# Optimization experiments

Measured on AMD Instinct MI355X. Metric: run time of the kernel, lower is better.

## Reference

```python
import jax, jax.numpy as jnp
import numpy as np
import math

D = 512; H = 4; HD = 128; S = 100; B = 32
HIN, WIN = 143, 111
HOUT, WOUT = 135, 103
FLAT = HIN * WIN  # 15873


def _pe():
    pos = np.arange(S, dtype=np.float32)[:, None]
    div = np.exp(np.arange(0, D, 2, dtype=np.float32) * (-math.log(10000.0) / D))
    pe = np.zeros((S, D), dtype=np.float32)
    pe[:, 0::2] = np.sin(pos * div)
    pe[:, 1::2] = np.cos(pos * div)
    return jnp.asarray(pe[:, None, :])  # (S,1,D)


def _pool_mat(n_in, n_out):
    # PyTorch AdaptiveAvgPool semantics: window [floor(i*in/out), ceil((i+1)*in/out))
    M = np.zeros((n_out, n_in), dtype=np.float32)
    for i in range(n_out):
        s = (i * n_in) // n_out
        e = -((-(i + 1) * n_in) // n_out)
        M[i, s:e] = 1.0 / (e - s)
    return jnp.asarray(M)


def _ln(x, g, b, eps=1e-5):
    m = jnp.mean(x, -1, keepdims=True)
    v = jnp.mean((x - m) ** 2, -1, keepdims=True)
    return (x - m) * jax.lax.rsqrt(v + eps) * g + b


def _mha(q_in, kv_in, qkv_w, qkv_b, pw, pb, key_pad):
    # q_in: (Sq,B,D), kv_in: (Sk,B,D); seq-first like nn.Transformer
    q = q_in @ qkv_w[:D].T + qkv_b[:D]
    k = kv_in @ qkv_w[D:2 * D].T + qkv_b[D:2 * D]
    v = kv_in @ qkv_w[2 * D:].T + qkv_b[2 * D:]
    Sq, Bb = q.shape[0], q.shape[1]
    Sk = k.shape[0]
    q = q.reshape(Sq, Bb, H, HD)
    k = k.reshape(Sk, Bb, H, HD)
    v = v.reshape(Sk, Bb, H, HD)
    sc = jnp.einsum('qbhd,kbhd->bhqk', q, k) / math.sqrt(HD)
    if key_pad is not None:
        sc = jnp.where(key_pad[:, None, None, :], -1e9, sc)
    a = jax.nn.softmax(sc, -1)
    o = jnp.einsum('bhqk,kbhd->qbhd', a, v).reshape(Sq, Bb, D)
    return o @ pw.T + pb


def _forward(x, fc1_w, fc1_b, fc2_w, fc2_b, fc3_w, fc3_b,
             out1_w, out1_b, out2_w, out2_b, out3_w, out3_b,
             enc_qkv_w, enc_qkv_b, enc_proj_w, enc_proj_b,
             enc_ff1_w, enc_ff1_b, enc_ff2_w, enc_ff2_b,
             enc_ln1_g, enc_ln1_b, enc_ln2_g, enc_ln2_b, enc_lnf_g, enc_lnf_b,
             dec_sa_qkv_w, dec_sa_qkv_b, dec_sa_proj_w, dec_sa_proj_b,
             dec_ca_qkv_w, dec_ca_qkv_b, dec_ca_proj_w, dec_ca_proj_b,
             dec_ff1_w, dec_ff1_b, dec_ff2_w, dec_ff2_b,
             dec_ln1_g, dec_ln1_b, dec_ln2_g, dec_ln2_b, dec_ln3_g, dec_ln3_b,
             dec_lnf_g, dec_lnf_b):
    Bb = x.shape[0]
    # Vectorized replacement of the per-sample torch.nonzero double loop:
    # padding[b,i] = True iff all timesteps k >= i are all-zero (and i >= 1).
    nz = jnp.any(x != 0, axis=(2, 3))  # (B,S)
    suffix_any = jnp.flip(jnp.cumsum(jnp.flip(nz, 1).astype(jnp.int32), 1), 1) > 0
    padding = (~suffix_any).at[:, 0].set(False)  # torch loop never touches step 0

    h = x.reshape(Bb * S, FLAT)
    h = jax.nn.relu(h @ fc1_w.T + fc1_b)
    h = jax.nn.relu(h @ fc2_w.T + fc2_b)
    h = jax.nn.relu(h @ fc3_w.T + fc3_b)
    h = h.reshape(Bb, S, D).transpose(1, 0, 2) + _pe()  # (S,B,D)

    for i in range(2):  # encoder, post-norm
        a = _mha(h, h, enc_qkv_w[i], enc_qkv_b[i], enc_proj_w[i], enc_proj_b[i], padding)
        h = _ln(h + a, enc_ln1_g[i], enc_ln1_b[i])
        f = jax.nn.relu(h @ enc_ff1_w[i].T + enc_ff1_b[i]) @ enc_ff2_w[i].T + enc_ff2_b[i]
        h = _ln(h + f, enc_ln2_g[i], enc_ln2_b[i])
    memory = _ln(h, enc_lnf_g, enc_lnf_b)

    t = jnp.ones((1, Bb, D), jnp.float32)  # trg
    for i in range(2):  # decoder, post-norm
        a = _mha(t, t, dec_sa_qkv_w[i], dec_sa_qkv_b[i], dec_sa_proj_w[i], dec_sa_proj_b[i], None)
        t = _ln(t + a, dec_ln1_g[i], dec_ln1_b[i])
        a = _mha(t, memory, dec_ca_qkv_w[i], dec_ca_qkv_b[i], dec_ca_proj_w[i], dec_ca_proj_b[i], None)
        t = _ln(t + a, dec_ln2_g[i], dec_ln2_b[i])
        f = jax.nn.relu(t @ dec_ff1_w[i].T + dec_ff1_b[i]) @ dec_ff2_w[i].T + dec_ff2_b[i]
        t = _ln(t + f, dec_ln3_g[i], dec_ln3_b[i])
    t = _ln(t, dec_lnf_g, dec_lnf_b)

    o = t[0]  # (B,512)
    o = jax.nn.relu(o @ out1_w.T + out1_b)
    o = jax.nn.relu(o @ out2_w.T + out2_b)
    o = jax.nn.relu(o @ out3_w.T + out3_b)
    o = o.reshape(Bb, HIN, WIN)
    return jnp.einsum('oh,bhw,pw->bop', _pool_mat(HIN, HOUT), o, _pool_mat(WIN, WOUT))


def setup_inputs() -> dict:
    key = jax.random.key(0)
    it = iter(jax.random.split(key, 48))

    def w(shape):
        return jax.random.normal(next(it), shape, jnp.float32) * 0.02

    x = jax.random.normal(next(it), (B, S, HIN, WIN), jnp.float32)
    lengths = jax.random.randint(next(it), (B,), 1, S + 1)
    keep = (jnp.arange(S)[None, :] < lengths[:, None]).astype(jnp.float32)
    x = x * keep[:, :, None, None]  # ragged: trailing timesteps are all-zero

    z, o1 = jnp.zeros, jnp.ones
    return dict(
        x=x,
        fc1_w=w((4096, FLAT)), fc1_b=z(4096),
        fc2_w=w((2048, 4096)), fc2_b=z(2048),
        fc3_w=w((D, 2048)), fc3_b=z(D),
        out1_w=w((2048, D)), out1_b=z(2048),
        out2_w=w((4096, 2048)), out2_b=z(4096),
        out3_w=w((FLAT, 4096)), out3_b=z(FLAT),
        enc_qkv_w=w((2, 3 * D, D)), enc_qkv_b=z((2, 3 * D)),
        enc_proj_w=w((2, D, D)), enc_proj_b=z((2, D)),
        enc_ff1_w=w((2, 1024, D)), enc_ff1_b=z((2, 1024)),
        enc_ff2_w=w((2, D, 1024)), enc_ff2_b=z((2, D)),
        enc_ln1_g=o1((2, D)), enc_ln1_b=z((2, D)),
        enc_ln2_g=o1((2, D)), enc_ln2_b=z((2, D)),
        enc_lnf_g=o1(D), enc_lnf_b=z(D),
        dec_sa_qkv_w=w((2, 3 * D, D)), dec_sa_qkv_b=z((2, 3 * D)),
        dec_sa_proj_w=w((2, D, D)), dec_sa_proj_b=z((2, D)),
        dec_ca_qkv_w=w((2, 3 * D, D)), dec_ca_qkv_b=z((2, 3 * D)),
        dec_ca_proj_w=w((2, D, D)), dec_ca_proj_b=z((2, D)),
        dec_ff1_w=w((2, 1024, D)), dec_ff1_b=z((2, 1024)),
        dec_ff2_w=w((2, D, 1024)), dec_ff2_b=z((2, D)),
        dec_ln1_g=o1((2, D)), dec_ln1_b=z((2, D)),
        dec_ln2_g=o1((2, D)), dec_ln2_b=z((2, D)),
        dec_ln3_g=o1((2, D)), dec_ln3_b=z((2, D)),
        dec_lnf_g=o1(D), dec_lnf_b=z(D),
    )


def reference(x, fc1_w, fc1_b, fc2_w, fc2_b, fc3_w, fc3_b,
              out1_w, out1_b, out2_w, out2_b, out3_w, out3_b,
              enc_qkv_w, enc_qkv_b, enc_proj_w, enc_proj_b,
              enc_ff1_w, enc_ff1_b, enc_ff2_w, enc_ff2_b,
              enc_ln1_g, enc_ln1_b, enc_ln2_g, enc_ln2_b, enc_lnf_g, enc_lnf_b,
              dec_sa_qkv_w, dec_sa_qkv_b, dec_sa_proj_w, dec_sa_proj_b,
              dec_ca_qkv_w, dec_ca_qkv_b, dec_ca_proj_w, dec_ca_proj_b,
              dec_ff1_w, dec_ff1_b, dec_ff2_w, dec_ff2_b,
              dec_ln1_g, dec_ln1_b, dec_ln2_g, dec_ln2_b, dec_ln3_g, dec_ln3_b,
              dec_lnf_g, dec_lnf_b):
    return _forward(x, fc1_w, fc1_b, fc2_w, fc2_b, fc3_w, fc3_b,
                    out1_w, out1_b, out2_w, out2_b, out3_w, out3_b,
                    enc_qkv_w, enc_qkv_b, enc_proj_w, enc_proj_b,
                    enc_ff1_w, enc_ff1_b, enc_ff2_w, enc_ff2_b,
                    enc_ln1_g, enc_ln1_b, enc_ln2_g, enc_ln2_b, enc_lnf_g, enc_lnf_b,
                    dec_sa_qkv_w, dec_sa_qkv_b, dec_sa_proj_w, dec_sa_proj_b,
                    dec_ca_qkv_w, dec_ca_qkv_b, dec_ca_proj_w, dec_ca_proj_b,
                    dec_ff1_w, dec_ff1_b, dec_ff2_w, dec_ff2_b,
                    dec_ln1_g, dec_ln1_b, dec_ln2_g, dec_ln2_b, dec_ln3_g, dec_ln3_b,
                    dec_lnf_g, dec_lnf_b)
```

## Files before the change

kernel.cpp:

```cpp
#include <hip/hip_runtime.h>
#include <hip/hip_bf16.h>

#define SEQ   100
#define BATCH 32
#define FLATIN 15873
#define KPAD1  16384
#define ROWS   3200
#define MPAD   3328
#define NOUT3  16000

typedef __attribute__((ext_vector_type(8))) short short8;
typedef __attribute__((ext_vector_type(4))) short short4v;
typedef __attribute__((ext_vector_type(4))) float f32x4;
typedef __hip_bfloat16 bf16;

__device__ __forceinline__ void gload_lds16(const void* g, void* l) {
  __builtin_amdgcn_global_load_lds((const __attribute__((address_space(1))) void*)g,
                                   (__attribute__((address_space(3))) void*)l, 16, 0, 0);
}

__device__ __forceinline__ int xcd_swizzle(int id, int nwg) {
  const int q = nwg >> 3, r = nwg & 7;
  const int x = id & 7, p = id >> 3;
  return (x < r ? x * (q + 1) : r * (q + 1) + (x - r) * q) + p;
}

#define GEMM_BODY(KBEG, KEND)                                                   \
  const int tid  = threadIdx.x;                                                 \
  const int lane = tid & 63;                                                    \
  const int wid  = tid >> 6;                                                    \
  const int wr = (wid >> 1) << 6;                                               \
  const int wc = (wid & 1) << 6;                                                \
  f32x4 acc[4][4];                                                              \
  _Pragma("unroll") for (int i = 0; i < 4; ++i)                                 \
  _Pragma("unroll") for (int j = 0; j < 4; ++j)                                 \
      acc[i][j] = (f32x4){0.f, 0.f, 0.f, 0.f};                                  \
  const int srow = (wid << 3) + (lane >> 3);                                    \
  const int scs  = lane & 7;                                                    \
  const int gcol = ((scs ^ (srow & 7)) << 3);                                   \
  const bf16* arow[4];                                                          \
  const bf16* brow[4];                                                          \
  _Pragma("unroll") for (int j = 0; j < 4; ++j) {                               \
    const int row = (j << 5) + srow;                                            \
    const int gr = GATHER ? idx[m0 + row] : (m0 + row);                         \
    arow[j] = A + (size_t)gr * K + gcol;                                        \
    brow[j] = W + (size_t)(n0 + row) * K + gcol;                                \
  }                                                                             \
  for (int k0 = (KBEG); k0 < (KEND); k0 += 64) {                                \
    __syncthreads();                                                            \
    _Pragma("unroll") for (int j = 0; j < 4; ++j) {                             \
      short* la = As + (((j << 2) + wid) << 9);                                 \
      short* lb = Bs + (((j << 2) + wid) << 9);                                 \
      gload_lds16(arow[j] + k0, la);                                            \
      gload_lds16(brow[j] + k0, lb);                                            \
    }                                                                           \
    __syncthreads();                                                            \
    _Pragma("unroll") for (int kk = 0; kk < 2; ++kk) {                          \
      short8 af[4], bfv[4];                                                     \
      _Pragma("unroll") for (int i = 0; i < 4; ++i) {                           \
        const int mr = wr + (i << 4) + (lane & 15);                             \
        const int cg = (kk << 2) + (lane >> 4);                                 \
        af[i]  = *(const short8*)(As + mr * 64 + ((cg ^ (mr & 7)) << 3));       \
        const int nr = wc + (i << 4) + (lane & 15);                             \
        bfv[i] = *(const short8*)(Bs + nr * 64 + ((cg ^ (nr & 7)) << 3));       \
      }                                                                         \
      _Pragma("unroll") for (int i = 0; i < 4; ++i)                             \
      _Pragma("unroll") for (int j = 0; j < 4; ++j)                             \
          acc[i][j] = __builtin_amdgcn_mfma_f32_16x16x32_bf16(af[i], bfv[j],    \
                                                              acc[i][j], 0,0,0);\
    }                                                                           \
  }

template<int GATHER>
__global__ __launch_bounds__(256)
void gemm_bf16(const bf16* __restrict__ A, const bf16* __restrict__ W,
               const int* __restrict__ idx, const int* __restrict__ cnt,
               float* __restrict__ P,
               int K, int ldc, int mtiles, int ksl, size_t pstride)
{
  __shared__ __align__(16) short lds[16384];
  short* As = lds;
  short* Bs = lds + 8192;
  const int wg = xcd_swizzle(blockIdx.x, gridDim.x);
  const int mt = wg % mtiles;
  const int g  = wg / mtiles;
  const int nt = g / ksl;
  const int ks = g % ksl;
  const int m0 = mt << 7;
  const int n0 = nt << 7;
  if (cnt && m0 >= cnt[0]) return;
  const int Klen = K / ksl;
  const int kbeg = ks * Klen;

  GEMM_BODY(kbeg, kbeg + Klen)

  float* Pout = P + (size_t)ks * pstride;
  const int fr = lane & 15, fq = lane >> 4;
#pragma unroll
  for (int j = 0; j < 4; ++j) {
    const int n = n0 + wc + (j << 4) + fr;
#pragma unroll
    for (int i = 0; i < 4; ++i)
#pragma unroll
      for (int r = 0; r < 4; ++r) {
        const int m = m0 + wr + (i << 4) + (fq << 2) + r;
        Pout[(size_t)m * ldc + n] = acc[i][j][r];
      }
  }
}

template<int RELU, int OF32, int OB16>
__global__ __launch_bounds__(256)
void gemm_direct(const bf16* __restrict__ A, const bf16* __restrict__ W,
                 const float* __restrict__ bias, float* __restrict__ Cf,
                 bf16* __restrict__ Cb, int K, int ldc, int mtiles)
{
  __shared__ __align__(16) short lds[16384];
  short* As = lds;
  short* Bs = lds + 8192;
  const int GATHER = 0;
  const int* idx = nullptr;
  const int wg = xcd_swizzle(blockIdx.x, gridDim.x);
  const int m0 = (wg % mtiles) << 7;
  const int n0 = (wg / mtiles) << 7;

  GEMM_BODY(0, K)

  const int fr = lane & 15, fq = lane >> 4;
#pragma unroll
  for (int j = 0; j < 4; ++j) {
    const int n = n0 + wc + (j << 4) + fr;
    const float bb = bias[n];
#pragma unroll
    for (int i = 0; i < 4; ++i)
#pragma unroll
      for (int r = 0; r < 4; ++r) {
        const int m = m0 + wr + (i << 4) + (fq << 2) + r;
        float v = acc[i][j][r] + bb;
        if (RELU) v = fmaxf(v, 0.f);
        if (OF32) Cf[(size_t)m * ldc + n] = v;
        if (OB16) Cb[(size_t)m * ldc + n] = __float2bfloat16(v);
      }
  }
}

__global__ __launch_bounds__(256)
void gemm_w32(const bf16* __restrict__ A, const float* __restrict__ W32,
              float* __restrict__ P, int K, int ldc, int ksl, size_t pstride,
              int wrows)
{
  __shared__ __align__(16) short lds[16384];
  short* As = lds;
  short* Bs = lds + 8192;
  const int wg = xcd_swizzle(blockIdx.x, gridDim.x);
  const int nt = wg / ksl;
  const int ks = wg % ksl;
  const int m0 = 0;
  const int n0 = nt << 7;
  const int Klen = K / ksl;
  const int kbeg = ks * Klen;
  const int kend = kbeg + Klen;

  const int tid  = threadIdx.x;
  const int lane = tid & 63;
  const int wid  = tid >> 6;
  const int wr = (wid >> 1) << 6;
  const int wc = (wid & 1) << 6;

  f32x4 acc[4][4];
#pragma unroll
  for (int i = 0; i < 4; ++i)
#pragma unroll
    for (int j = 0; j < 4; ++j) acc[i][j] = (f32x4){0.f, 0.f, 0.f, 0.f};

  const int srow = (wid << 3) + (lane >> 3);
  const int scs  = lane & 7;
  const int gcol = ((scs ^ (srow & 7)) << 3);

  const bf16* arow[4];
#pragma unroll
  for (int j = 0; j < 4; ++j)
    arow[j] = A + (size_t)(m0 + (j << 5) + srow) * K + gcol;

  const float* wsrc[4];
  int bslot[4];
#pragma unroll
  for (int i = 0; i < 4; ++i) {
    const int q = (i << 8) + tid;
    const int row = q >> 3, c = q & 7;
    const int wrow = min(n0 + row, wrows - 1);
    wsrc[i] = W32 + (size_t)wrow * K + (c << 3);
    bslot[i] = row * 64 + ((c ^ (row & 7)) << 3);
  }

  for (int k0 = kbeg; k0 < kend; k0 += 64) {
    __syncthreads();
#pragma unroll
    for (int j = 0; j < 4; ++j)
      gload_lds16(arow[j] + k0, As + (((j << 2) + wid) << 9));
#pragma unroll
    for (int i = 0; i < 4; ++i) {
      const float4 w0 = *(const float4*)(wsrc[i] + k0);
      const float4 w1 = *(const float4*)(wsrc[i] + k0 + 4);
      union { short8 v; bf16 h[8]; } pk;
      pk.h[0] = __float2bfloat16(w0.x); pk.h[1] = __float2bfloat16(w0.y);
      pk.h[2] = __float2bfloat16(w0.z); pk.h[3] = __float2bfloat16(w0.w);
      pk.h[4] = __float2bfloat16(w1.x); pk.h[5] = __float2bfloat16(w1.y);
      pk.h[6] = __float2bfloat16(w1.z); pk.h[7] = __float2bfloat16(w1.w);
      *(short8*)(Bs + bslot[i]) = pk.v;
    }
    __syncthreads();
#pragma unroll
    for (int kk = 0; kk < 2; ++kk) {
      short8 af[4], bfv[4];
#pragma unroll
      for (int i = 0; i < 4; ++i) {
        const int mr = wr + (i << 4) + (lane & 15);
        const int cg = (kk << 2) + (lane >> 4);
        af[i]  = *(const short8*)(As + mr * 64 + ((cg ^ (mr & 7)) << 3));
        const int nr = wc + (i << 4) + (lane & 15);
        bfv[i] = *(const short8*)(Bs + nr * 64 + ((cg ^ (nr & 7)) << 3));
      }
#pragma unroll
      for (int i = 0; i < 4; ++i)
#pragma unroll
        for (int j = 0; j < 4; ++j)
          acc[i][j] = __builtin_amdgcn_mfma_f32_16x16x32_bf16(af[i], bfv[j], acc[i][j], 0, 0, 0);
    }
  }

  float* Pout = P + (size_t)ks * pstride;
  const int fr = lane & 15, fq = lane >> 4;
#pragma unroll
  for (int j = 0; j < 4; ++j) {
    const int n = n0 + wc + (j << 4) + fr;
#pragma unroll
    for (int i = 0; i < 4; ++i)
#pragma unroll
      for (int r = 0; r < 4; ++r) {
        const int m = m0 + wr + (i << 4) + (fq << 2) + r;
        Pout[(size_t)m * ldc + n] = acc[i][j][r];
      }
  }
}

template<int RELU, int OF32, int OB16>
__global__ __launch_bounds__(256)
void reduce_kernel(const float* __restrict__ P, size_t pstride, int ksl,
                   const float* __restrict__ bias, float* __restrict__ Cf,
                   bf16* __restrict__ Cb, int N, const int* __restrict__ cnt)
{
  const int row = blockIdx.y;
  if (cnt) { const int cp = (cnt[0] + 127) & ~127; if (row >= cp) return; }
  const int n = (blockIdx.x * 256 + threadIdx.x) * 4;
  if (n >= N) return;
  const size_t o = (size_t)row * N + n;
  const float4 b4 = *(const float4*)(bias + n);
  float4 s = *(const float4*)(P + o);
  for (int k = 1; k < ksl; ++k) {
    const float4 p = *(const float4*)(P + (size_t)k * pstride + o);
    s.x += p.x; s.y += p.y; s.z += p.z; s.w += p.w;
  }
  s.x += b4.x; s.y += b4.y; s.z += b4.z; s.w += b4.w;
  if (RELU) {
    s.x = fmaxf(s.x, 0.f); s.y = fmaxf(s.y, 0.f);
    s.z = fmaxf(s.z, 0.f); s.w = fmaxf(s.w, 0.f);
  }
  if (OF32) *(float4*)(Cf + o) = s;
  if (OB16) {
    union { short4v v; bf16 h[4]; } u;
    u.h[0] = __float2bfloat16(s.x);
    u.h[1] = __float2bfloat16(s.y);
    u.h[2] = __float2bfloat16(s.z);
    u.h[3] = __float2bfloat16(s.w);
    *(short4v*)(Cb + o) = u.v;
  }
}

__global__ __launch_bounds__(256)
void conv_x_kernel(const float* __restrict__ x, bf16* __restrict__ xb,
                   int* __restrict__ nz)
{
  __shared__ int sred[4];
  const int m = blockIdx.x;
  const int t = threadIdx.x;
  bf16* dst = xb + (size_t)m * KPAD1;
  if (m == ROWS) {
    const __hip_bfloat162 z2 = {__float2bfloat16(0.f), __float2bfloat16(0.f)};
    for (int c = t; c < (KPAD1 >> 1); c += 256) *(__hip_bfloat162*)(dst + 2 * c) = z2;
    return;
  }
  const float* src = x + (size_t)m * FLATIN;
  int any = 0;
  for (int c = t; c < (KPAD1 >> 1); c += 256) {
    const int c0 = 2 * c;
    const float v0 = (c0 < FLATIN) ? src[c0] : 0.f;
    const float v1 = (c0 + 1 < FLATIN) ? src[c0 + 1] : 0.f;
    any |= (v0 != 0.f) | (v1 != 0.f);
    __hip_bfloat162 pr;
    pr.x = __float2bfloat16(v0);
    pr.y = __float2bfloat16(v1);
    *(__hip_bfloat162*)(dst + c0) = pr;
  }
  any = __any(any) ? 1 : 0;
  if ((t & 63) == 0) sred[t >> 6] = any;
  __syncthreads();
  if (t == 0) nz[m] = sred[0] | sred[1] | sred[2] | sred[3];
}

__global__ __launch_bounds__(256)
void compact_kernel(const int* __restrict__ nz, int* __restrict__ idx,
                    int* __restrict__ pos, int* __restrict__ cnt,
                    int* __restrict__ pad,
                    const float* __restrict__ dkvb, float* __restrict__ kvbias)
{
  __shared__ int wsum[4];
  __shared__ int total;
  const int t = threadIdx.x;
  int loc[13];
  int c = 0;
#pragma unroll
  for (int i = 0; i < 13; ++i) {
    const int m = t * 13 + i;
    loc[i] = (m < ROWS) ? nz[m] : 0;
    c += loc[i];
  }
  int v = c;
#pragma unroll
  for (int o = 1; o < 64; o <<= 1) {
    const int u = __shfl_up(v, o);
    if ((t & 63) >= o) v += u;
  }
  if ((t & 63) == 63) wsum[t >> 6] = v;
  __syncthreads();
  int wbase = 0;
  for (int w = 0; w < (t >> 6); ++w) wbase += wsum[w];
  int p = wbase + v - c;
#pragma unroll
  for (int i = 0; i < 13; ++i) {
    const int m = t * 13 + i;
    if (m < ROWS) {
      if (loc[i]) { idx[p] = m; pos[m] = p; ++p; }
      else pos[m] = -1;
    }
  }
  if (t == 255) total = p;
  __syncthreads();
  const int count = total;
  if (t == 0) cnt[0] = count + 1;
  for (int i = count + t; i < MPAD; i += 256) idx[i] = ROWS;
  for (int m = t; m < ROWS; m += 256) if (pos[m] < 0) pos[m] = count;
  if (t < 32) {
    int any = 0;
    for (int s = 99; s >= 0; --s) {
      any |= nz[t * 100 + s];
      pad[t * 100 + s] = (s > 0 && !any) ? 1 : 0;
    }
  }
#pragma unroll
  for (int i = t; i < 2048; i += 256) {
    const int L = i >> 10, j = i & 1023;
    kvbias[i] = dkvb[L * 1536 + 512 + j];
  }
}

struct CvtArgs {
  const float* src[8];
  bf16* dst[8];
  int cum[8];
};
struct TrArgs {
  const float* src[13];
  float* dst[13];
  int R[13], C[13], cum[13];
};
struct PrepArgs {
  CvtArgs cv;
  TrArgs tr;
  const float* fc1w;
  bf16* wb1;
  int nCvt, nFc1;
};
__global__ __launch_bounds__(256)
void prep_kernel(PrepArgs a)
{
  __shared__ float tbuf[64][65];
  const int bid0 = blockIdx.x;
  if (bid0 < a.nCvt) {
    const int bid = bid0;
    int seg = 0;
#pragma unroll
    for (int i = 1; i < 8; ++i) if (bid >= a.cv.cum[i]) seg = i;
    const size_t e0 = ((size_t)(bid - a.cv.cum[seg]) << 11) + (threadIdx.x << 3);
    const float4 v0 = *(const float4*)(a.cv.src[seg] + e0);
    const float4 v1 = *(const float4*)(a.cv.src[seg] + e0 + 4);
    union { short8 v; bf16 h[8]; } pk;
    pk.h[0] = __float2bfloat16(v0.x); pk.h[1] = __float2bfloat16(v0.y);
    pk.h[2] = __float2bfloat16(v0.z); pk.h[3] = __float2bfloat16(v0.w);
    pk.h[4] = __float2bfloat16(v1.x); pk.h[5] = __float2bfloat16(v1.y);
    pk.h[6] = __float2bfloat16(v1.z); pk.h[7] = __float2bfloat16(v1.w);
    *(short8*)(a.cv.dst[seg] + e0) = pk.v;
  } else if (bid0 < a.nCvt + a.nFc1) {
    const int r = bid0 - a.nCvt;
    const float* src = a.fc1w + (size_t)r * FLATIN;
    bf16* dst = a.wb1 + (size_t)r * KPAD1;
#pragma unroll
    for (int u = 0; u < KPAD1 / 2048; ++u) {
      const int c0 = u * 2048 + threadIdx.x * 8;
      union { short8 v; bf16 h[8]; } pk;
      if (c0 + 8 <= FLATIN) {
        const float4 p = *(const float4*)(src + c0);
        const float4 q = *(const float4*)(src + c0 + 4);
        pk.h[0] = __float2bfloat16(p.x); pk.h[1] = __float2bfloat16(p.y);
        pk.h[2] = __float2bfloat16(p.z); pk.h[3] = __float2bfloat16(p.w);
        pk.h[4] = __float2bfloat16(q.x); pk.h[5] = __float2bfloat16(q.y);
        pk.h[6] = __float2bfloat16(q.z); pk.h[7] = __float2bfloat16(q.w);
      } else {
#pragma unroll
        for (int i = 0; i < 8; ++i)
          pk.h[i] = __float2bfloat16((c0 + i < FLATIN) ? src[c0 + i] : 0.f);
      }
      *(short8*)(dst + c0) = pk.v;
    }
  } else {
    const int bid = bid0 - a.nCvt - a.nFc1;
    int seg = 0;
#pragma unroll
    for (int i = 1; i < 13; ++i) if (bid >= a.tr.cum[i]) seg = i;
    const int local = bid - a.tr.cum[seg];
    const int R = a.tr.R[seg], C = a.tr.C[seg];
    const int tilesC = C >> 6;
    const int r0 = (local / tilesC) << 6;
    const int c0 = (local % tilesC) << 6;
    const int tx = threadIdx.x & 63, ty = threadIdx.x >> 6;
    const float* s = a.tr.src[seg];
    float* d = a.tr.dst[seg];
#pragma unroll
    for (int i = 0; i < 16; ++i) {
      const int rr = (ty << 4) + i;
      tbuf[rr][tx] = s[(size_t)(r0 + rr) * C + c0 + tx];
    }
    __syncthreads();
#pragma unroll
    for (int i = 0; i < 16; ++i) {
      const int cc = (ty << 4) + i;
      d[(size_t)(c0 + cc) * R + r0 + tx] = tbuf[tx][cc];
    }
  }
}

__global__ __launch_bounds__(256)
void scatter_pe_reduce(const float* __restrict__ P, size_t pstride, int ksl,
                       const int* __restrict__ pos, const float* __restrict__ bias,
                       float* __restrict__ hf, bf16* __restrict__ hb)
{
  const int m = blockIdx.x;
  const int s = m % 100, b = m / 100;
  const int src = pos[m];
  const int t = threadIdx.x;
  const size_t sb = (size_t)src * 512;
  const size_t db = (size_t)(s * 32 + b) * 512;
#pragma unroll
  for (int u = 0; u < 2; ++u) {
    const int d = t + u * 256;
    float v = bias[d];
    for (int k = 0; k < ksl; ++k) v += P[(size_t)k * pstride + sb + d];
    const float div = expf((float)(2 * (d >> 1)) * (-9.210340371976184f / 512.f));
    const float arg = (float)s * div;
    const float pe = (d & 1) ? cosf(arg) : sinf(arg);
    v = fmaxf(v, 0.f) + pe;
    hf[db + d] = v;
    hb[db + d] = __float2bfloat16(v);
  }
}

__global__ __launch_bounds__(256)
void ln_kernel(const float* __restrict__ x, const float* __restrict__ res,
               const float* __restrict__ g, const float* __restrict__ bta,
               const float* __restrict__ gf, const float* __restrict__ bf_,
               int dofinal, float* __restrict__ y, bf16* __restrict__ yb)
{
  __shared__ float rs[4], rss[4];
  const int row = blockIdx.x;
  const int t = threadIdx.x;
  const size_t base = (size_t)row * 512;
  float v0 = x[base + t];
  float v1 = x[base + t + 256];
  if (res) { v0 += res[base + t]; v1 += res[base + t + 256]; }
  float o0, o1;
#pragma unroll
  for (int pass = 0; pass < 2; ++pass) {
    float s = v0 + v1, ss = v0 * v0 + v1 * v1;
#pragma unroll
    for (int o = 32; o > 0; o >>= 1) { s += __shfl_xor(s, o); ss += __shfl_xor(ss, o); }
    if ((t & 63) == 0) { rs[t >> 6] = s; rss[t >> 6] = ss; }
    __syncthreads();
    s = rs[0] + rs[1] + rs[2] + rs[3];
    ss = rss[0] + rss[1] + rss[2] + rss[3];
    __syncthreads();
    const float mean = s * (1.f / 512.f);
    const float var = ss * (1.f / 512.f) - mean * mean;
    const float inv = rsqrtf(var + 1e-5f);
    const float* gg = (pass == 0) ? g : gf;
    const float* bb = (pass == 0) ? bta : bf_;
    o0 = (v0 - mean) * inv * gg[t] + bb[t];
    o1 = (v1 - mean) * inv * gg[t + 256] + bb[t + 256];
    if (pass == 1 || !dofinal) break;
    v0 = o0; v1 = o1;
  }
  if (y) {
    y[base + t] = o0;
    y[base + t + 256] = o1;
  }
  if (yb) {
    yb[base + t] = __float2bfloat16(o0);
    yb[base + t + 256] = __float2bfloat16(o1);
  }
}

__global__ __launch_bounds__(256)
void enc_attn_kernel(const float* __restrict__ qkv, const int* __restrict__ pad,
                     bf16* __restrict__ ob)
{
  __shared__ float Ks[100][129];
  __shared__ float Qs[128];
  __shared__ float Ps[100];
  __shared__ float red[4];
  const int bh = blockIdx.x;
  const int b = bh >> 2, h = bh & 3;
  const int q0 = blockIdx.y * 4;
  const int t = threadIdx.x;
  for (int i = t; i < 12800; i += 256) {
    const int s = i >> 7, d = i & 127;
    Ks[s][d] = qkv[(size_t)(s * 32 + b) * 1536 + 512 + h * 128 + d];
  }
  const int masked = (t < 100) ? pad[b * 100 + t] : 0;
  const float scale = 0.08838834764831845f;
  for (int qi = 0; qi < 4; ++qi) {
    const int q = q0 + qi;
    __syncthreads();
    if (t < 128) Qs[t] = qkv[(size_t)(q * 32 + b) * 1536 + h * 128 + t];
    __syncthreads();
    float sc = -3e38f;
    if (t < 100) {
      const float* kr = &Ks[t][0];
      float a = 0.f;
#pragma unroll 16
      for (int d = 0; d < 128; ++d) a += Qs[d] * kr[d];
      sc = masked ? -1e9f : (a * scale);
    }
    float mx = sc;
#pragma unroll
    for (int o = 32; o > 0; o >>= 1) mx = fmaxf(mx, __shfl_xor(mx, o));
    if ((t & 63) == 0) red[t >> 6] = mx;
    __syncthreads();
    mx = fmaxf(fmaxf(red[0], red[1]), fmaxf(red[2], red[3]));
    const float e = (t < 100) ? expf(sc - mx) : 0.f;
    float sm = e;
#pragma unroll
    for (int o = 32; o > 0; o >>= 1) sm += __shfl_xor(sm, o);
    __syncthreads();
    if ((t & 63) == 0) red[t >> 6] = sm;
    __syncthreads();
    sm = red[0] + red[1] + red[2] + red[3];
    if (t < 100) Ps[t] = e;
    __syncthreads();
    if (t < 128) {
      float a = 0.f;
      const float* vb = qkv + 1024 + h * 128 + t;
      for (int k = 0; k < 100; ++k) a += Ps[k] * vb[(size_t)(k * 32 + b) * 1536];
      ob[(size_t)(q * 32 + b) * 512 + h * 128 + t] = __float2bfloat16(a / sm);
    }
  }
}

template<int N, int K, int RELU>
__device__ __forceinline__ void gemvT(int tid, const float* S,
                                      const float* __restrict__ WT,
                                      const float* __restrict__ bias,
                                      float* out, float* part)
{
  constexpr int NQ = N / 4;
  constexpr int G = 512 / NQ;
  constexpr int KP = K / G;
  const int p = tid % NQ;
  const int g = tid / NQ;
  const float4* wp = (const float4*)WT;
  float ax = 0.f, ay = 0.f, az = 0.f, aw = 0.f;
  const int kend = g * KP + KP;
#pragma unroll 8
  for (int k = g * KP; k < kend; ++k) {
    const float s = S[k];
    const float4 w = wp[(size_t)k * NQ + p];
    ax += s * w.x; ay += s * w.y; az += s * w.z; aw += s * w.w;
  }
  float4 a4 = {ax, ay, az, aw};
  *(float4*)(part + g * N + 4 * p) = a4;
  __syncthreads();
#pragma unroll
  for (int n = tid; n < N; n += 512) {
    float v = bias[n];
#pragma unroll
    for (int q = 0; q < G; ++q) v += part[q * N + n];
    if (RELU) v = fmaxf(v, 0.f);
    out[n] = v;
  }
  __syncthreads();
}

#define BLOCK_LN512(V, G, B, O)                                                 \
  {                                                                             \
    float s_ = (V), ss_ = (V) * (V);                                            \
    _Pragma("unroll")                                                           \
    for (int o_ = 32; o_ > 0; o_ >>= 1) {                                       \
      s_ += __shfl_xor(s_, o_); ss_ += __shfl_xor(ss_, o_);                     \
    }                                                                           \
    if ((tid & 63) == 0) { red[tid >> 6] = s_; red2[tid >> 6] = ss_; }          \
    __syncthreads();                                                            \
    s_ = 0.f; ss_ = 0.f;                                                        \
    _Pragma("unroll")                                                           \
    for (int w_ = 0; w_ < 8; ++w_) { s_ += red[w_]; ss_ += red2[w_]; }          \
    const float mean_ = s_ * (1.f / 512.f);                                     \
    const float inv_ = rsqrtf(ss_ * (1.f / 512.f) - mean_ * mean_ + 1e-5f);     \
    O = ((V) - mean_) * inv_ * (G)[tid] + (B)[tid];                             \
    __syncthreads();                                                            \
  }

__global__ __launch_bounds__(512)
void dec_layer(const float* __restrict__ tin,
               const float* __restrict__ kvb, int kvstride,
               const float* __restrict__ WvT, const float* __restrict__ bv,
               const float* __restrict__ WpT, const float* __restrict__ bp,
               const float* __restrict__ g1, const float* __restrict__ b1,
               const float* __restrict__ WqT, const float* __restrict__ bq,
               const float* __restrict__ WcpT, const float* __restrict__ bcp,
               const float* __restrict__ g2, const float* __restrict__ b2,
               const float* __restrict__ W1T, const float* __restrict__ b1f,
               const float* __restrict__ W2T, const float* __restrict__ b2f,
               const float* __restrict__ g3, const float* __restrict__ b3,
               const float* __restrict__ gf, const float* __restrict__ bf_,
               int dofinal, float* __restrict__ tout,
               const float* __restrict__ Wo1T, const float* __restrict__ ob1,
               bf16* __restrict__ o1b)
{
  __shared__ float Ts[512], Bs[512], Cs[512], F1[1024], part[2048];
  __shared__ float Ps[4][104];
  __shared__ float red[8], red2[8];
  const int r = blockIdx.x, tid = threadIdx.x;
  Ts[tid] = tin ? tin[r * 512 + tid] : 1.0f;
  __syncthreads();

  gemvT<512, 512, 0>(tid, Ts, WvT, bv, Bs, part);
  gemvT<512, 512, 0>(tid, Bs, WpT, bp, Cs, part);
  {
    const float rr = Cs[tid] + Ts[tid];
    float o;
    BLOCK_LN512(rr, g1, b1, o)
    Ts[tid] = o;
  }
  __syncthreads();

  gemvT<512, 512, 0>(tid, Ts, WqT, bq, Bs, part);

  if (tid < 256) {
    const int h = tid >> 6, lane = tid & 63;
    const float scale = 0.08838834764831845f;
    const float* Qh = Bs + h * 128;
    float s0, s1 = -3e38f;
    {
      const float* kr = kvb + (size_t)(lane * 32 + r) * kvstride + h * 128;
      float a = 0.f;
#pragma unroll 16
      for (int d = 0; d < 128; ++d) a += Qh[d] * kr[d];
      s0 = a * scale;
    }
    if (lane + 64 < 100) {
      const float* kr = kvb + (size_t)((lane + 64) * 32 + r) * kvstride + h * 128;
      float a = 0.f;
#pragma unroll 16
      for (int d = 0; d < 128; ++d) a += Qh[d] * kr[d];
      s1 = a * scale;
    }
    float mx = fmaxf(s0, s1);
#pragma unroll
    for (int o = 32; o > 0; o >>= 1) mx = fmaxf(mx, __shfl_xor(mx, o));
    const float e0 = expf(s0 - mx);
    const float e1 = (lane + 64 < 100) ? expf(s1 - mx) : 0.f;
    float sm = e0 + e1;
#pragma unroll
    for (int o = 32; o > 0; o >>= 1) sm += __shfl_xor(sm, o);
    Ps[h][lane] = e0 / sm;
    if (lane + 64 < 100) Ps[h][lane + 64] = e1 / sm;
  }
  __syncthreads();
  if (tid < 256) {
    const int h = tid >> 6, lane = tid & 63;
#pragma unroll
    for (int u = 0; u < 2; ++u) {
      const int d = lane + u * 64;
      const float* vb = kvb + 512 + h * 128 + d;
      float a = 0.f;
      for (int k = 0; k < 100; ++k) a += Ps[h][k] * vb[(size_t)(k * 32 + r) * kvstride];
      Bs[h * 128 + d] = a;
    }
  }
  __syncthreads();

  gemvT<512, 512, 0>(tid, Bs, WcpT, bcp, Cs, part);
  {
    const float rr = Cs[tid] + Ts[tid];
    float o;
    BLOCK_LN512(rr, g2, b2, o)
    Ts[tid] = o;
  }
  __syncthreads();

  gemvT<1024, 512, 1>(tid, Ts, W1T, b1f, F1, part);
  gemvT<512, 1024, 0>(tid, F1, W2T, b2f, Cs, part);
  {
    const float rr = Cs[tid] + Ts[tid];
    float o;
    BLOCK_LN512(rr, g3, b3, o)
    if (dofinal) {
      float f;
      BLOCK_LN512(o, gf, bf_, f)
      o = f;
    }
    tout[r * 512 + tid] = o;
    if (dofinal) {
      Ts[tid] = o;
      __syncthreads();
      const float4* wp = (const float4*)Wo1T;
      float ax = 0.f, ay = 0.f, az = 0.f, aw = 0.f;
#pragma unroll 8
      for (int k = 0; k < 512; ++k) {
        const float s = Ts[k];
        const float4 w = wp[(size_t)k * 512 + tid];
        ax += s * w.x; ay += s * w.y; az += s * w.z; aw += s * w.w;
      }
      union { short4v v; bf16 h[4]; } u;
      u.h[0] = __float2bfloat16(fmaxf(ax + ob1[4 * tid], 0.f));
      u.h[1] = __float2bfloat16(fmaxf(ay + ob1[4 * tid + 1], 0.f));
      u.h[2] = __float2bfloat16(fmaxf(az + ob1[4 * tid + 2], 0.f));
      u.h[3] = __float2bfloat16(fmaxf(aw + ob1[4 * tid + 3], 0.f));
      *(short4v*)(o1b + (size_t)r * 2048 + 4 * tid) = u.v;
      const short4v z = {0, 0, 0, 0};
#pragma unroll
      for (int rr = r + 32; rr < 128; rr += 32)
        *(short4v*)(o1b + (size_t)rr * 2048 + 4 * tid) = z;
    }
  }
}

__global__ __launch_bounds__(256)
void reduce_pool(const float* __restrict__ P, size_t pstride,
                 const float* __restrict__ bias, float* __restrict__ out)
{
  __shared__ float row[NOUT3];
  const int b = blockIdx.x, t = threadIdx.x;
  for (int n = t * 4; n < NOUT3; n += 1024) {
    const size_t o = (size_t)b * NOUT3 + n;
    float4 s = *(const float4*)(P + o);
#pragma unroll
    for (int k = 1; k < 4; ++k) {
      const float4 p = *(const float4*)(P + (size_t)k * pstride + o);
      s.x += p.x; s.y += p.y; s.z += p.z; s.w += p.w;
    }
    row[n]     = fmaxf(s.x + ((n     < FLATIN) ? bias[n]     : 0.f), 0.f);
    row[n + 1] = fmaxf(s.y + ((n + 1 < FLATIN) ? bias[n + 1] : 0.f), 0.f);
    row[n + 2] = fmaxf(s.z + ((n + 2 < FLATIN) ? bias[n + 2] : 0.f), 0.f);
    row[n + 3] = fmaxf(s.w + ((n + 3 < FLATIN) ? bias[n + 3] : 0.f), 0.f);
  }
  __syncthreads();
  for (int i = t; i < 135 * 103; i += 256) {
    const int j = i % 103, r = i / 103;
    const int rs = (r * 143) / 135, re = ((r + 1) * 143 + 134) / 135;
    const int cs = (j * 111) / 103, ce = ((j + 1) * 111 + 102) / 103;
    float s = 0.f;
    for (int rr = rs; rr < re; ++rr)
      for (int cc = cs; cc < ce; ++cc)
        s += row[rr * 111 + cc];
    out[(size_t)b * (135 * 103) + i] = s / (float)((re - rs) * (ce - cs));
  }
}

extern "C" void kernel_launch(void* const* d_in, const int* in_sizes, int n_in,
                              void* d_out, int out_size, void* d_ws, size_t ws_size,
                              hipStream_t stream)
{
  (void)in_sizes; (void)n_in; (void)out_size; (void)ws_size;

  const float* x          = (const float*)d_in[0];
  const float* fc1_w      = (const float*)d_in[1];
  const float* fc1_b      = (const float*)d_in[2];
  const float* fc2_w      = (const float*)d_in[3];
  const float* fc2_b      = (const float*)d_in[4];
  const float* fc3_w      = (const float*)d_in[5];
  const float* fc3_b      = (const float*)d_in[6];
  const float* out1_w     = (const float*)d_in[7];
  const float* out1_b     = (const float*)d_in[8];
  const float* out2_w     = (const float*)d_in[9];
  const float* out2_b     = (const float*)d_in[10];
  const float* out3_w     = (const float*)d_in[11];
  const float* out3_b     = (const float*)d_in[12];
  const float* enc_qkv_w  = (const float*)d_in[13];
  const float* enc_qkv_b  = (const float*)d_in[14];
  const float* enc_proj_w = (const float*)d_in[15];
  const float* enc_proj_b = (const float*)d_in[16];
  const float* enc_ff1_w  = (const float*)d_in[17];
  const float* enc_ff1_b  = (const float*)d_in[18];
  const float* enc_ff2_w  = (const float*)d_in[19];
  const float* enc_ff2_b  = (const float*)d_in[20];
  const float* enc_ln1_g  = (const float*)d_in[21];
  const float* enc_ln1_b  = (const float*)d_in[22];
  const float* enc_ln2_g  = (const float*)d_in[23];
  const float* enc_ln2_b  = (const float*)d_in[24];
  const float* enc_lnf_g  = (const float*)d_in[25];
  const float* enc_lnf_b  = (const float*)d_in[26];
  const float* dec_sa_qkv_w  = (const float*)d_in[27];
  const float* dec_sa_qkv_b  = (const float*)d_in[28];
  const float* dec_sa_proj_w = (const float*)d_in[29];
  const float* dec_sa_proj_b = (const float*)d_in[30];
  const float* dec_ca_qkv_w  = (const float*)d_in[31];
  const float* dec_ca_qkv_b  = (const float*)d_in[32];
  const float* dec_ca_proj_w = (const float*)d_in[33];
  const float* dec_ca_proj_b = (const float*)d_in[34];
  const float* dec_ff1_w  = (const float*)d_in[35];
  const float* dec_ff1_b  = (const float*)d_in[36];
  const float* dec_ff2_w  = (const float*)d_in[37];
  const float* dec_ff2_b  = (const float*)d_in[38];
  const float* dec_ln1_g  = (const float*)d_in[39];
  const float* dec_ln1_b  = (const float*)d_in[40];
  const float* dec_ln2_g  = (const float*)d_in[41];
  const float* dec_ln2_b  = (const float*)d_in[42];
  const float* dec_ln3_g  = (const float*)d_in[43];
  const float* dec_ln3_b  = (const float*)d_in[44];
  const float* dec_lnf_g  = (const float*)d_in[45];
  const float* dec_lnf_b  = (const float*)d_in[46];

  char* wsp = (char*)d_ws;
  size_t off = 0;
  auto alloc = [&](size_t nbytes) -> char* {
    char* p = wsp + off;
    off += (nbytes + 255) & ~(size_t)255;
    return p;
  };

  bf16* xb     = (bf16*)alloc((size_t)MPAD * KPAD1 * 2);
  bf16* Wb1    = (bf16*)alloc((size_t)4096 * KPAD1 * 2);
  bf16* Wb2    = (bf16*)alloc((size_t)2048 * 4096 * 2);
  bf16* Wb3    = (bf16*)alloc((size_t)512 * 2048 * 2);
  bf16* Wqkvb  = (bf16*)alloc((size_t)2 * 1536 * 512 * 2);
  bf16* Wprojb = (bf16*)alloc((size_t)2 * 512 * 512 * 2);
  bf16* Wff1b  = (bf16*)alloc((size_t)2 * 1024 * 512 * 2);
  bf16* Wff2b  = (bf16*)alloc((size_t)2 * 512 * 1024 * 2);
  bf16* Wkv2b  = (bf16*)alloc((size_t)2048 * 512 * 2);
  int*   nz      = (int*)alloc(ROWS * 4);
  int*   padmask = (int*)alloc(ROWS * 4);
  int*   idx     = (int*)alloc(MPAD * 4);
  int*   pos     = (int*)alloc(ROWS * 4);
  int*   cnt     = (int*)alloc(256);
  float* kvbias  = (float*)alloc(2048 * 4);
  bf16* h1c = (bf16*)alloc((size_t)MPAD * 4096 * 2);
  bf16* h2c = (bf16*)alloc((size_t)MPAD * 2048 * 2);
  float* hf  = (float*)alloc((size_t)ROWS * 512 * 4);
  bf16* hb = (bf16*)alloc((size_t)ROWS * 512 * 2);
  float* qkvbuf = (float*)alloc((size_t)ROWS * 1536 * 4);
  bf16* attnb = (bf16*)alloc((size_t)ROWS * 512 * 2);
  float* pjf  = (float*)alloc((size_t)ROWS * 512 * 4);
  bf16* f1b = (bf16*)alloc((size_t)ROWS * 1024 * 2);
  float* f2f  = (float*)alloc((size_t)ROWS * 512 * 4);
  bf16* memb = (bf16*)alloc((size_t)ROWS * 512 * 2);
  float* kv01 = (float*)alloc((size_t)ROWS * 2048 * 4);
  float* tbuf = (float*)alloc(32 * 512 * 4);
  float* WvT[2]  = { (float*)alloc(512 * 512 * 4), (float*)alloc(512 * 512 * 4) };
  float* WpT[2]  = { (float*)alloc(512 * 512 * 4), (float*)alloc(512 * 512 * 4) };
  float* WqT[2]  = { (float*)alloc(512 * 512 * 4), (float*)alloc(512 * 512 * 4) };
  float* WcpT[2] = { (float*)alloc(512 * 512 * 4), (float*)alloc(512 * 512 * 4) };
  float* W1T[2]  = { (float*)alloc(512 * 1024 * 4), (float*)alloc(512 * 1024 * 4) };
  float* W2T[2]  = { (float*)alloc(1024 * 512 * 4), (float*)alloc(1024 * 512 * 4) };
  float* Wo1T    = (float*)alloc((size_t)512 * 2048 * 4);
  float* fcP  = (float*)alloc((size_t)4 * MPAD * 4096 * 4);
  float* encP = (float*)alloc((size_t)2 * ROWS * 1536 * 4);

  float* outP = fcP;
  bf16* o1b  = (bf16*)((char*)encP + ((size_t)20 << 20));
  bf16* o2b  = (bf16*)((char*)encP + ((size_t)22 << 20));

  const size_t psF1 = (size_t)MPAD * 4096;
  const size_t psF2 = (size_t)MPAD * 2048;
  const size_t psF3 = (size_t)MPAD * 512;

  conv_x_kernel<<<ROWS + 1, 256, 0, stream>>>(x, xb, nz);
  compact_kernel<<<1, 256, 0, stream>>>(nz, idx, pos, cnt, padmask,
                                        dec_ca_qkv_b, kvbias);
  {
    PrepArgs pa;
    const float* srcs[8] = { enc_qkv_w, enc_proj_w, enc_ff1_w, enc_ff2_w,
                             dec_ca_qkv_w + (size_t)512 * 512,
                             dec_ca_qkv_w + (size_t)(1536 + 512) * 512,
                             fc2_w, fc3_w };
    bf16* dsts[8] = { Wqkvb, Wprojb, Wff1b, Wff2b,
                      Wkv2b, Wkv2b + (size_t)1024 * 512, Wb2, Wb3 };
    const int counts[8] = { 2*1536*512, 2*512*512, 2*1024*512, 2*512*1024,
                            1024*512, 1024*512, 2048*4096, 512*2048 };
    int c = 0;
    for (int i = 0; i < 8; ++i) { pa.cv.src[i] = srcs[i]; pa.cv.dst[i] = dsts[i];
                                  pa.cv.cum[i] = c; c += counts[i] >> 11; }
    pa.nCvt = c;
    pa.fc1w = fc1_w; pa.wb1 = Wb1; pa.nFc1 = 4096;
    const float* tsr[13];
    float* tds[13];
    int R[13], C[13];
    int n = 0;
    for (int L = 0; L < 2; ++L) {
      tsr[n] = dec_sa_qkv_w + (size_t)L * 1536 * 512 + (size_t)1024 * 512;
      tds[n] = WvT[L]; R[n] = 512; C[n] = 512; ++n;
      tsr[n] = dec_sa_proj_w + (size_t)L * 512 * 512;
      tds[n] = WpT[L]; R[n] = 512; C[n] = 512; ++n;
      tsr[n] = dec_ca_qkv_w + (size_t)L * 1536 * 512;
      tds[n] = WqT[L]; R[n] = 512; C[n] = 512; ++n;
      tsr[n] = dec_ca_proj_w + (size_t)L * 512 * 512;
      tds[n] = WcpT[L]; R[n] = 512; C[n] = 512; ++n;
      tsr[n] = dec_ff1_w + (size_t)L * 1024 * 512;
      tds[n] = W1T[L]; R[n] = 1024; C[n] = 512; ++n;
      tsr[n] = dec_ff2_w + (size_t)L * 512 * 1024;
      tds[n] = W2T[L]; R[n] = 512; C[n] = 1024; ++n;
    }
    tsr[n] = out1_w; tds[n] = Wo1T; R[n] = 2048; C[n] = 512; ++n;
    int tc = 0;
    for (int i = 0; i < 13; ++i) {
      pa.tr.src[i] = tsr[i]; pa.tr.dst[i] = tds[i];
      pa.tr.R[i] = R[i]; pa.tr.C[i] = C[i];
      pa.tr.cum[i] = tc; tc += (R[i] >> 6) * (C[i] >> 6);
    }
    prep_kernel<<<pa.nCvt + pa.nFc1 + tc, 256, 0, stream>>>(pa);
  }

  gemm_bf16<1><<<26 * 32 * 2, 256, 0, stream>>>(xb, Wb1, idx, cnt, fcP,
      KPAD1, 4096, 26, 2, psF1);
  reduce_kernel<1, 0, 1><<<dim3(4, MPAD), 256, 0, stream>>>(fcP, psF1, 2,
      fc1_b, nullptr, h1c, 4096, cnt);
  gemm_bf16<0><<<26 * 16 * 4, 256, 0, stream>>>(h1c, Wb2, nullptr, cnt, fcP,
      4096, 2048, 26, 4, psF2);
  reduce_kernel<1, 0, 1><<<dim3(2, MPAD), 256, 0, stream>>>(fcP, psF2, 4,
      fc2_b, nullptr, h2c, 2048, cnt);
  gemm_bf16<0><<<26 * 4 * 4, 256, 0, stream>>>(h2c, Wb3, nullptr, cnt, fcP,
      2048, 512, 26, 4, psF3);
  scatter_pe_reduce<<<ROWS, 256, 0, stream>>>(fcP, psF3, 4, pos, fc3_b, hf, hb);

  for (int L = 0; L < 2; ++L) {
    gemm_direct<0, 1, 0><<<25 * 12, 256, 0, stream>>>(hb, Wqkvb + (size_t)L * 1536 * 512,
        enc_qkv_b + L * 1536, qkvbuf, nullptr, 512, 1536, 25);
    enc_attn_kernel<<<dim3(128, 25), 256, 0, stream>>>(qkvbuf, padmask, attnb);
    gemm_direct<0, 1, 0><<<25 * 4, 256, 0, stream>>>(attnb, Wprojb + (size_t)L * 512 * 512,
        enc_proj_b + L * 512, pjf, nullptr, 512, 512, 25);
    ln_kernel<<<ROWS, 256, 0, stream>>>(hf, pjf, enc_ln1_g + L * 512, enc_ln1_b + L * 512,
        nullptr, nullptr, 0, hf, hb);
    gemm_direct<1, 0, 1><<<25 * 8, 256, 0, stream>>>(hb, Wff1b + (size_t)L * 1024 * 512,
        enc_ff1_b + L * 1024, nullptr, f1b, 512, 1024, 25);
    gemm_direct<0, 1, 0><<<25 * 4, 256, 0, stream>>>(f1b, Wff2b + (size_t)L * 512 * 1024,
        enc_ff2_b + L * 512, f2f, nullptr, 1024, 512, 25);
    if (L == 0) {
      ln_kernel<<<ROWS, 256, 0, stream>>>(hf, f2f, enc_ln2_g, enc_ln2_b,
          nullptr, nullptr, 0, hf, hb);
    } else {
      ln_kernel<<<ROWS, 256, 0, stream>>>(hf, f2f, enc_ln2_g + 512, enc_ln2_b + 512,
          enc_lnf_g, enc_lnf_b, 1, nullptr, memb);
    }
  }

  gemm_direct<0, 1, 0><<<25 * 16, 256, 0, stream>>>(memb, Wkv2b, kvbias,
      kv01, nullptr, 512, 2048, 25);

  for (int L = 0; L < 2; ++L) {
    dec_layer<<<32, 512, 0, stream>>>(
        (L == 0) ? nullptr : tbuf,
        kv01 + (size_t)L * 1024, 2048,
        WvT[L], dec_sa_qkv_b + L * 1536 + 1024,
        WpT[L], dec_sa_proj_b + L * 512,
        dec_ln1_g + L * 512, dec_ln1_b + L * 512,
        WqT[L], dec_ca_qkv_b + L * 1536,
        WcpT[L], dec_ca_proj_b + L * 512,
        dec_ln2_g + L * 512, dec_ln2_b + L * 512,
        W1T[L], dec_ff1_b + L * 1024,
        W2T[L], dec_ff2_b + L * 512,
        dec_ln3_g + L * 512, dec_ln3_b + L * 512,
        dec_lnf_g, dec_lnf_b, (L == 1) ? 1 : 0, tbuf,
        Wo1T, out1_b, o1b);
  }

  gemm_w32<<<32 * 4, 256, 0, stream>>>(o1b, out2_w, outP,
      2048, 4096, 4, (size_t)128 * 4096, 4096);
  reduce_kernel<1, 0, 1><<<dim3(4, 128), 256, 0, stream>>>(outP, (size_t)128 * 4096, 4,
      out2_b, nullptr, o2b, 4096, nullptr);
  gemm_w32<<<125 * 4, 256, 0, stream>>>(o2b, out3_w, outP,
      4096, NOUT3, 4, (size_t)128 * NOUT3, FLATIN);
  reduce_pool<<<32, 256, 0, stream>>>(outP, (size_t)128 * NOUT3, out3_b, (float*)d_out);
}
```

Baseline: 1.389 ms.

## Fuse input conversion into prep kernel and store transposed decoder weights in bf16

Moves the x-to-bf16 conversion and nonzero-row detection into the combined prep kernel, which drops a separate launch and lets that work overlap with the weight conversion blocks. The compaction kernel now runs after prep. The transposed decoder and output weights are now stored as bf16 instead of fp32, halving the bytes the decoder GEMV loops read. Decoder arithmetic now uses bf16-rounded weights, which costs some precision.

```diff
diff --git a/kernel.cpp b/kernel.cpp
--- a/kernel.cpp
+++ b/kernel.cpp
@@ -278,37 +278,6 @@
 }
 
 __global__ __launch_bounds__(256)
-void conv_x_kernel(const float* __restrict__ x, bf16* __restrict__ xb,
-                   int* __restrict__ nz)
-{
-  __shared__ int sred[4];
-  const int m = blockIdx.x;
-  const int t = threadIdx.x;
-  bf16* dst = xb + (size_t)m * KPAD1;
-  if (m == ROWS) {
-    const __hip_bfloat162 z2 = {__float2bfloat16(0.f), __float2bfloat16(0.f)};
-    for (int c = t; c < (KPAD1 >> 1); c += 256) *(__hip_bfloat162*)(dst + 2 * c) = z2;
-    return;
-  }
-  const float* src = x + (size_t)m * FLATIN;
-  int any = 0;
-  for (int c = t; c < (KPAD1 >> 1); c += 256) {
-    const int c0 = 2 * c;
-    const float v0 = (c0 < FLATIN) ? src[c0] : 0.f;
-    const float v1 = (c0 + 1 < FLATIN) ? src[c0 + 1] : 0.f;
-    any |= (v0 != 0.f) | (v1 != 0.f);
-    __hip_bfloat162 pr;
-    pr.x = __float2bfloat16(v0);
-    pr.y = __float2bfloat16(v1);
-    *(__hip_bfloat162*)(dst + c0) = pr;
-  }
-  any = __any(any) ? 1 : 0;
-  if ((t & 63) == 0) sred[t >> 6] = any;
-  __syncthreads();
-  if (t == 0) nz[m] = sred[0] | sred[1] | sred[2] | sred[3];
-}
-
-__global__ __launch_bounds__(256)
 void compact_kernel(const int* __restrict__ nz, int* __restrict__ idx,
                     int* __restrict__ pos, int* __restrict__ cnt,
                     int* __restrict__ pad,
@@ -371,23 +340,52 @@
 };
 struct TrArgs {
   const float* src[13];
-  float* dst[13];
+  bf16* dst[13];
   int R[13], C[13], cum[13];
 };
 struct PrepArgs {
   CvtArgs cv;
   TrArgs tr;
+  const float* x;
+  bf16* xb;
+  int* nz;
   const float* fc1w;
   bf16* wb1;
-  int nCvt, nFc1;
+  int nConv, nCvt, nFc1;
 };
 __global__ __launch_bounds__(256)
 void prep_kernel(PrepArgs a)
 {
   __shared__ float tbuf[64][65];
+  __shared__ int sred[4];
   const int bid0 = blockIdx.x;
-  if (bid0 < a.nCvt) {
-    const int bid = bid0;
+  if (bid0 < a.nConv) {
+    const int m = bid0;
+    const int t = threadIdx.x;
+    bf16* dst = a.xb + (size_t)m * KPAD1;
+    if (m == ROWS) {
+      const __hip_bfloat162 z2 = {__float2bfloat16(0.f), __float2bfloat16(0.f)};
+      for (int c = t; c < (KPAD1 >> 1); c += 256) *(__hip_bfloat162*)(dst + 2 * c) = z2;
+      return;
+    }
+    const float* src = a.x + (size_t)m * FLATIN;
+    int any = 0;
+    for (int c = t; c < (KPAD1 >> 1); c += 256) {
+      const int c0 = 2 * c;
+      const float v0 = (c0 < FLATIN) ? src[c0] : 0.f;
+      const float v1 = (c0 + 1 < FLATIN) ? src[c0 + 1] : 0.f;
+      any |= (v0 != 0.f) | (v1 != 0.f);
+      __hip_bfloat162 pr;
+      pr.x = __float2bfloat16(v0);
+      pr.y = __float2bfloat16(v1);
+      *(__hip_bfloat162*)(dst + c0) = pr;
+    }
+    any = __any(any) ? 1 : 0;
+    if ((t & 63) == 0) sred[t >> 6] = any;
+    __syncthreads();
+    if (t == 0) a.nz[m] = sred[0] | sred[1] | sred[2] | sred[3];
+  } else if (bid0 < a.nConv + a.nCvt) {
+    const int bid = bid0 - a.nConv;
     int seg = 0;
 #pragma unroll
     for (int i = 1; i < 8; ++i) if (bid >= a.cv.cum[i]) seg = i;
@@ -400,8 +398,8 @@
     pk.h[4] = __float2bfloat16(v1.x); pk.h[5] = __float2bfloat16(v1.y);
     pk.h[6] = __float2bfloat16(v1.z); pk.h[7] = __float2bfloat16(v1.w);
     *(short8*)(a.cv.dst[seg] + e0) = pk.v;
-  } else if (bid0 < a.nCvt + a.nFc1) {
-    const int r = bid0 - a.nCvt;
+  } else if (bid0 < a.nConv + a.nCvt + a.nFc1) {
+    const int r = bid0 - a.nConv - a.nCvt;
     const float* src = a.fc1w + (size_t)r * FLATIN;
     bf16* dst = a.wb1 + (size_t)r * KPAD1;
 #pragma unroll
@@ -423,7 +421,7 @@
       *(short8*)(dst + c0) = pk.v;
     }
   } else {
-    const int bid = bid0 - a.nCvt - a.nFc1;
+    const int bid = bid0 - a.nConv - a.nCvt - a.nFc1;
     int seg = 0;
 #pragma unroll
     for (int i = 1; i < 13; ++i) if (bid >= a.tr.cum[i]) seg = i;
@@ -434,7 +432,7 @@
     const int c0 = (local % tilesC) << 6;
     const int tx = threadIdx.x & 63, ty = threadIdx.x >> 6;
     const float* s = a.tr.src[seg];
-    float* d = a.tr.dst[seg];
+    bf16* d = a.tr.dst[seg];
 #pragma unroll
     for (int i = 0; i < 16; ++i) {
       const int rr = (ty << 4) + i;
@@ -444,7 +442,7 @@
 #pragma unroll
     for (int i = 0; i < 16; ++i) {
       const int cc = (ty << 4) + i;
-      d[(size_t)(c0 + cc) * R + r0 + tx] = tbuf[tx][cc];
+      d[(size_t)(c0 + cc) * R + r0 + tx] = __float2bfloat16(tbuf[tx][cc]);
     }
   }
 }
@@ -576,7 +574,7 @@
 
 template<int N, int K, int RELU>
 __device__ __forceinline__ void gemvT(int tid, const float* S,
-                                      const float* __restrict__ WT,
+                                      const bf16* __restrict__ WT,
                                       const float* __restrict__ bias,
                                       float* out, float* part)
 {
@@ -585,14 +583,18 @@
   constexpr int KP = K / G;
   const int p = tid % NQ;
   const int g = tid / NQ;
-  const float4* wp = (const float4*)WT;
+  const short4v* wp = (const short4v*)WT;
   float ax = 0.f, ay = 0.f, az = 0.f, aw = 0.f;
   const int kend = g * KP + KP;
 #pragma unroll 8
   for (int k = g * KP; k < kend; ++k) {
     const float s = S[k];
-    const float4 w = wp[(size_t)k * NQ + p];
-    ax += s * w.x; ay += s * w.y; az += s * w.z; aw += s * w.w;
+    union { short4v v; bf16 h[4]; } w;
+    w.v = wp[(size_t)k * NQ + p];
+    ax += s * __bfloat162float(w.h[0]);
+    ay += s * __bfloat162float(w.h[1]);
+    az += s * __bfloat162float(w.h[2]);
+    aw += s * __bfloat162float(w.h[3]);
   }
   float4 a4 = {ax, ay, az, aw};
   *(float4*)(part + g * N + 4 * p) = a4;
@@ -629,18 +631,18 @@
 __global__ __launch_bounds__(512)
 void dec_layer(const float* __restrict__ tin,
                const float* __restrict__ kvb, int kvstride,
-               const float* __restrict__ WvT, const float* __restrict__ bv,
-               const float* __restrict__ WpT, const float* __restrict__ bp,
+               const bf16* __restrict__ WvT, const float* __restrict__ bv,
+               const bf16* __restrict__ WpT, const float* __restrict__ bp,
                const float* __restrict__ g1, const float* __restrict__ b1,
-               const float* __restrict__ WqT, const float* __restrict__ bq,
-               const float* __restrict__ WcpT, const float* __restrict__ bcp,
+               const bf16* __restrict__ WqT, const float* __restrict__ bq,
+               const bf16* __restrict__ WcpT, const float* __restrict__ bcp,
                const float* __restrict__ g2, const float* __restrict__ b2,
-               const float* __restrict__ W1T, const float* __restrict__ b1f,
-               const float* __restrict__ W2T, const float* __restrict__ b2f,
+               const bf16* __restrict__ W1T, const float* __restrict__ b1f,
+               const bf16* __restrict__ W2T, const float* __restrict__ b2f,
                const float* __restrict__ g3, const float* __restrict__ b3,
                const float* __restrict__ gf, const float* __restrict__ bf_,
                int dofinal, float* __restrict__ tout,
-               const float* __restrict__ Wo1T, const float* __restrict__ ob1,
+               const bf16* __restrict__ Wo1T, const float* __restrict__ ob1,
                bf16* __restrict__ o1b)
 {
   __shared__ float Ts[512], Bs[512], Cs[512], F1[1024], part[2048];
@@ -730,13 +732,17 @@
     if (dofinal) {
       Ts[tid] = o;
       __syncthreads();
-      const float4* wp = (const float4*)Wo1T;
+      const short4v* wp = (const short4v*)Wo1T;
       float ax = 0.f, ay = 0.f, az = 0.f, aw = 0.f;
 #pragma unroll 8
       for (int k = 0; k < 512; ++k) {
         const float s = Ts[k];
-        const float4 w = wp[(size_t)k * 512 + tid];
-        ax += s * w.x; ay += s * w.y; az += s * w.z; aw += s * w.w;
+        union { short4v v; bf16 h[4]; } w;
+        w.v = wp[(size_t)k * 512 + tid];
+        ax += s * __bfloat162float(w.h[0]);
+        ay += s * __bfloat162float(w.h[1]);
+        az += s * __bfloat162float(w.h[2]);
+        aw += s * __bfloat162float(w.h[3]);
       }
       union { short4v v; bf16 h[4]; } u;
       u.h[0] = __float2bfloat16(fmaxf(ax + ob1[4 * tid], 0.f));
@@ -873,13 +879,13 @@
   bf16* memb = (bf16*)alloc((size_t)ROWS * 512 * 2);
   float* kv01 = (float*)alloc((size_t)ROWS * 2048 * 4);
   float* tbuf = (float*)alloc(32 * 512 * 4);
-  float* WvT[2]  = { (float*)alloc(512 * 512 * 4), (float*)alloc(512 * 512 * 4) };
-  float* WpT[2]  = { (float*)alloc(512 * 512 * 4), (float*)alloc(512 * 512 * 4) };
-  float* WqT[2]  = { (float*)alloc(512 * 512 * 4), (float*)alloc(512 * 512 * 4) };
-  float* WcpT[2] = { (float*)alloc(512 * 512 * 4), (float*)alloc(512 * 512 * 4) };
-  float* W1T[2]  = { (float*)alloc(512 * 1024 * 4), (float*)alloc(512 * 1024 * 4) };
-  float* W2T[2]  = { (float*)alloc(1024 * 512 * 4), (float*)alloc(1024 * 512 * 4) };
-  float* Wo1T    = (float*)alloc((size_t)512 * 2048 * 4);
+  bf16* WvT[2]  = { (bf16*)alloc(512 * 512 * 2), (bf16*)alloc(512 * 512 * 2) };
+  bf16* WpT[2]  = { (bf16*)alloc(512 * 512 * 2), (bf16*)alloc(512 * 512 * 2) };
+  bf16* WqT[2]  = { (bf16*)alloc(512 * 512 * 2), (bf16*)alloc(512 * 512 * 2) };
+  bf16* WcpT[2] = { (bf16*)alloc(512 * 512 * 2), (bf16*)alloc(512 * 512 * 2) };
+  bf16* W1T[2]  = { (bf16*)alloc(512 * 1024 * 2), (bf16*)alloc(512 * 1024 * 2) };
+  bf16* W2T[2]  = { (bf16*)alloc(1024 * 512 * 2), (bf16*)alloc(1024 * 512 * 2) };
+  bf16* Wo1T    = (bf16*)alloc((size_t)512 * 2048 * 2);
   float* fcP  = (float*)alloc((size_t)4 * MPAD * 4096 * 4);
   float* encP = (float*)alloc((size_t)2 * ROWS * 1536 * 4);
 
@@ -891,11 +897,9 @@
   const size_t psF2 = (size_t)MPAD * 2048;
   const size_t psF3 = (size_t)MPAD * 512;
 
-  conv_x_kernel<<<ROWS + 1, 256, 0, stream>>>(x, xb, nz);
-  compact_kernel<<<1, 256, 0, stream>>>(nz, idx, pos, cnt, padmask,
-                                        dec_ca_qkv_b, kvbias);
   {
     PrepArgs pa;
+    pa.x = x; pa.xb = xb; pa.nz = nz; pa.nConv = ROWS + 1;
     const float* srcs[8] = { enc_qkv_w, enc_proj_w, enc_ff1_w, enc_ff2_w,
                              dec_ca_qkv_w + (size_t)512 * 512,
                              dec_ca_qkv_w + (size_t)(1536 + 512) * 512,
@@ -910,7 +914,7 @@
     pa.nCvt = c;
     pa.fc1w = fc1_w; pa.wb1 = Wb1; pa.nFc1 = 4096;
     const float* tsr[13];
-    float* tds[13];
+    bf16* tds[13];
     int R[13], C[13];
     int n = 0;
     for (int L = 0; L < 2; ++L) {
@@ -934,8 +938,10 @@
       pa.tr.R[i] = R[i]; pa.tr.C[i] = C[i];
       pa.tr.cum[i] = tc; tc += (R[i] >> 6) * (C[i] >> 6);
     }
-    prep_kernel<<<pa.nCvt + pa.nFc1 + tc, 256, 0, stream>>>(pa);
-  }
+    prep_kernel<<<pa.nConv + pa.nCvt + pa.nFc1 + tc, 256, 0, stream>>>(pa);
+  }
+  compact_kernel<<<1, 256, 0, stream>>>(nz, idx, pos, cnt, padmask,
+                                        dec_ca_qkv_b, kvbias);
 
   gemm_bf16<1><<<26 * 32 * 2, 256, 0, stream>>>(xb, Wb1, idx, cnt, fcP,
       KPAD1, 4096, 26, 2, psF1);
```

Result: faster. 1.301 ms (-6.3%).
